# Performance work log

Measured on AMD Instinct MI355X. Metric: run time of the kernel, lower is better.

Reference implementation:

```python
import jax, jax.numpy as jnp
import numpy as np

B, C, H, W = 128, 512, 14, 14
WIN, SHIFT = 7, 3
HEADS, HD = 16, 32
HID = 2048
EPS = 1e-5
N = WIN * WIN
NWH = H // WIN
NW = NWH * NWH


def _rel_pos_index():
    coords = np.stack(np.meshgrid(np.arange(WIN), np.arange(WIN), indexing='ij'))  # (2,Wh,Ww)
    flat = coords.reshape(2, -1)
    rel = (flat[:, :, None] - flat[:, None, :]).transpose(1, 2, 0)  # (N,N,2)
    rel[..., 0] += WIN - 1
    rel[..., 1] += WIN - 1
    rel[..., 0] *= 2 * WIN - 1
    return rel.sum(-1)  # (N,N) in [0, (2W-1)^2)


def _attn_mask():
    img = np.zeros((H, W))
    cnt = 0
    for h in (slice(0, -WIN), slice(-WIN, -SHIFT), slice(-SHIFT, None)):
        for w in (slice(0, -WIN), slice(-WIN, -SHIFT), slice(-SHIFT, None)):
            img[h, w] = cnt
            cnt += 1
    mw = img.reshape(NWH, WIN, NWH, WIN).transpose(0, 2, 1, 3).reshape(-1, N)  # (nW,N)
    d = mw[:, None, :] - mw[:, :, None]
    return np.where(d != 0, -100.0, 0.0).astype(np.float32)  # (nW,N,N)


REL_IDX = _rel_pos_index()
ATTN_MASK = jnp.asarray(_attn_mask())


def _ln_c(x, w, b):
    # LayerNorm2d: normalize over channel dim of NCHW
    mu = x.mean(axis=1, keepdims=True)
    var = ((x - mu) ** 2).mean(axis=1, keepdims=True)
    xn = (x - mu) * jax.lax.rsqrt(var + EPS)
    return xn * w[None, :, None, None] + b[None, :, None, None]


def setup_inputs() -> dict:
    key = jax.random.key(0)
    ks = jax.random.split(key, 12)
    s = 0.02
    return {
        'x': jax.random.normal(ks[0], (B, C, H, W), jnp.float32),
        'ln1_w': jnp.ones((C,), jnp.float32),
        'ln1_b': jnp.zeros((C,), jnp.float32),
        'qkv_w': jax.random.normal(ks[1], (3 * C, C), jnp.float32) * s,
        'qkv_b': jnp.zeros((3 * C,), jnp.float32),
        'rel_bias': jax.random.normal(ks[2], ((2 * WIN - 1) ** 2, HEADS), jnp.float32) * s,
        'proj_w': jax.random.normal(ks[3], (C, C), jnp.float32) * s,
        'proj_b': jnp.zeros((C,), jnp.float32),
        'gamma1': jnp.full((C,), 1e-6, jnp.float32),
        'ln2_w': jnp.ones((C,), jnp.float32),
        'ln2_b': jnp.zeros((C,), jnp.float32),
        'fc1_w': jax.random.normal(ks[4], (HID, C), jnp.float32) * s,
        'fc1_b': jnp.zeros((HID,), jnp.float32),
        'fc2_w': jax.random.normal(ks[5], (C, HID), jnp.float32) * s,
        'fc2_b': jnp.zeros((C,), jnp.float32),
        'gamma2': jnp.full((C,), 1e-6, jnp.float32),
    }


def reference(x, ln1_w, ln1_b, qkv_w, qkv_b, rel_bias, proj_w, proj_b, gamma1,
              ln2_w, ln2_b, fc1_w, fc1_b, fc2_w, fc2_b, gamma2):
    # ---- shifted-window attention branch ----
    y = _ln_c(x, ln1_w, ln1_b).transpose(0, 2, 3, 1)  # (B,H,W,C)
    y = jnp.roll(y, (-SHIFT, -SHIFT), axis=(1, 2))
    # window partition -> (B*nW, N, C)
    xw = y.reshape(B, NWH, WIN, NWH, WIN, C).transpose(0, 1, 3, 2, 4, 5).reshape(B * NW, N, C)
    qkv = (xw @ qkv_w.T + qkv_b).reshape(B * NW, N, 3, HEADS, HD).transpose(2, 0, 3, 1, 4)
    q, k, v = qkv[0], qkv[1], qkv[2]  # (B*nW, heads, N, hd)
    attn = jnp.einsum('bhnd,bhmd->bhnm', q * (HD ** -0.5), k)
    bias = rel_bias[REL_IDX.reshape(-1)].reshape(N, N, HEADS).transpose(2, 0, 1)  # (heads,N,N)
    attn = attn + bias[None]
    attn = attn.reshape(B, NW, HEADS, N, N) + ATTN_MASK[None, :, None]
    attn = jax.nn.softmax(attn.reshape(B * NW, HEADS, N, N), axis=-1)
    out = jnp.einsum('bhnm,bhmd->bhnd', attn, v).transpose(0, 2, 1, 3).reshape(B * NW, N, C)
    out = out @ proj_w.T + proj_b
    # window reverse + roll back
    y = out.reshape(B, NWH, NWH, WIN, WIN, C).transpose(0, 1, 3, 2, 4, 5).reshape(B, H, W, C)
    y = jnp.roll(y, (SHIFT, SHIFT), axis=(1, 2))
    y = gamma1 * y  # layer scale over channel (last dim in NHWC)
    x = x + y.transpose(0, 3, 1, 2)
    # ---- MLP branch ----
    z = _ln_c(x, ln2_w, ln2_b).transpose(0, 2, 3, 1)  # (B,H,W,C)
    z = jax.nn.gelu(z @ fc1_w.T + fc1_b, approximate=False)
    z = z @ fc2_w.T + fc2_b
    z = gamma2 * z
    return x + z.transpose(0, 3, 1, 2)
```

## Files before the change

kernel.cpp:

```cpp
#include <hip/hip_runtime.h>
#include <cmath>
#include <cstdint>

typedef float floatx4 __attribute__((ext_vector_type(4)));

#define EPS_ 1e-5f
#define QSCALE 0.17677669529663689f

__device__ __forceinline__ void gload16(const uint8_t* g, uint8_t* l) {
  __builtin_amdgcn_global_load_lds(
      (const __attribute__((address_space(1))) void*)g,
      (__attribute__((address_space(3))) void*)l, 16, 0, 0);
}

template<bool HI>
__device__ __forceinline__ int pk_fp8(float a, float b, int old) {
  return __builtin_amdgcn_cvt_pk_fp8_f32(a, b, old, HI);
}
__device__ __forceinline__ int pk_fp8x4(float v0, float v1, float v2, float v3) {
  int w = pk_fp8<false>(v0, v1, 0);
  return pk_fp8<true>(v2, v3, w);
}

__device__ __forceinline__ uint16_t f2bf(float f) {
  uint32_t u = __float_as_uint(f);
  return (uint16_t)((u + 0x7fffu + ((u >> 16) & 1u)) >> 16);
}
__device__ __forceinline__ float bf2f(uint16_t h) {
  return __uint_as_float(((uint32_t)h) << 16);
}


template<int K>
__global__ void cvt_frag(const float* __restrict__ s, uint8_t* __restrict__ d, int n4) {
  const int i = blockIdx.x * 256 + threadIdx.x;
  if (i >= n4) return;
  const int kq = K >> 2;
  const int n = i / kq;
  const int k = (i - n * kq) << 2;
  const float4 v = ((const float4*)s)[i];
  const int panel = ((n >> 6) << 2) + (n & 3);
  const int lm = (n >> 2) & 15;
  const long addr = (long)panel * (16 * K) + ((k >> 3) << 7) + (lm << 3) + (k & 4);
  *(int*)(d + addr) = pk_fp8x4(v.x, v.y, v.z, v.w);
}

__global__ __launch_bounds__(256)
void ln_stats_nchw(const float* __restrict__ x, float* __restrict__ mu, float* __restrict__ rs) {
  const int tl = threadIdx.x & 63;
  const int wv = threadIdx.x >> 6;
  const int t = blockIdx.x * 64 + tl;
  const int b = t / 196;
  const int p = t - b * 196;
  const float* xp = x + (long)b * 100352 + p;
  float s = 0.f, ss = 0.f;
  const int cbeg = wv * 128;
  for (int c = cbeg; c < cbeg + 128; ++c) {
    const float v = xp[(long)c * 196];
    s += v; ss += v * v;
  }
  __shared__ float sb[4][64], qb[4][64];
  sb[wv][tl] = s; qb[wv][tl] = ss;
  __syncthreads();
  if (wv == 0) {
    s  = sb[0][tl] + sb[1][tl] + sb[2][tl] + sb[3][tl];
    ss = qb[0][tl] + qb[1][tl] + qb[2][tl] + qb[3][tl];
    const float m = s * (1.f / 512.f);
    const float var = ss * (1.f / 512.f) - m * m;
    mu[t] = m;
    rs[t] = rsqrtf(var + EPS_);
  }
}

__global__ __launch_bounds__(256)
void ln1_apply(const float* __restrict__ x, const float* __restrict__ mu, const float* __restrict__ rs,
               const float* __restrict__ w, const float* __restrict__ bb, uint8_t* __restrict__ A) {
  __shared__ float tile[64][53];
  const int bid = blockIdx.x;
  const int ct = bid & 7;
  const int pt = (bid >> 3) & 3;
  const int b = bid >> 5;
  const int p0 = pt * 49, c0 = ct * 64;
  const long xbase = (long)b * 100352;
  for (int idx = threadIdx.x; idx < 3136; idx += 256) {
    const int cl = idx / 49;
    const int pl = idx - cl * 49;
    tile[cl][pl] = x[xbase + (long)(c0 + cl) * 196 + p0 + pl];
  }
  __syncthreads();
  const int tbase = b * 196 + p0;
  for (int idx = threadIdx.x; idx < 784; idx += 256) {
    const int pl = idx >> 4;
    const int cq = (idx & 15) << 2;
    const int t = tbase + pl;
    const int c = c0 + cq;
    const float m = mu[t], rr = rs[t];
    const float v0 = (tile[cq + 0][pl] - m) * rr * w[c + 0] + bb[c + 0];
    const float v1 = (tile[cq + 1][pl] - m) * rr * w[c + 1] + bb[c + 1];
    const float v2 = (tile[cq + 2][pl] - m) * rr * w[c + 2] + bb[c + 2];
    const float v3 = (tile[cq + 3][pl] - m) * rr * w[c + 3] + bb[c + 3];
    const long addr = (long)(t & ~15) * 512 + ((c >> 3) << 7) + ((t & 15) << 3) + (c & 4);
    *(int*)(A + addr) = pk_fp8x4(v0, v1, v2, v3);
  }
}

__global__ __launch_bounds__(256)
void ln2_panel(const uint16_t* __restrict__ Xb, const float* __restrict__ S1,
               const float* __restrict__ S2, const float* __restrict__ w,
               const float* __restrict__ bb, uint8_t* __restrict__ Z) {
  __shared__ float xs[16 * 516];
  const int p = blockIdx.x;
  const int t0 = p * 16;
  for (int idx = threadIdx.x; idx < 1024; idx += 256) {
    const int tl = idx >> 6;
    const int c8 = (idx & 63) << 3;
    const uint4 raw = *(const uint4*)(Xb + ((long)(t0 + tl) << 9) + c8);
    float* xr = xs + tl * 516 + c8;
    xr[0] = bf2f((uint16_t)(raw.x & 0xffff)); xr[1] = bf2f((uint16_t)(raw.x >> 16));
    xr[2] = bf2f((uint16_t)(raw.y & 0xffff)); xr[3] = bf2f((uint16_t)(raw.y >> 16));
    xr[4] = bf2f((uint16_t)(raw.z & 0xffff)); xr[5] = bf2f((uint16_t)(raw.z >> 16));
    xr[6] = bf2f((uint16_t)(raw.w & 0xffff)); xr[7] = bf2f((uint16_t)(raw.w >> 16));
  }
  __syncthreads();
  uint8_t* zp = Z + (long)p * 8192;
  for (int e = threadIdx.x; e < 2048; e += 256) {
    const int off = e << 2;
    const int k8 = off >> 7;
    const int tl = (off >> 3) & 15;
    const int c = (k8 << 3) + (off & 4);
    const int t = t0 + tl;
    const float m = S1[t] * (1.f / 512.f);
    const float var = S2[t] * (1.f / 512.f) - m * m;
    const float r = rsqrtf(var + EPS_);
    const float* xr = xs + tl * 516 + c;
    const float v0 = (xr[0] - m) * r * w[c + 0] + bb[c + 0];
    const float v1 = (xr[1] - m) * r * w[c + 1] + bb[c + 1];
    const float v2 = (xr[2] - m) * r * w[c + 2] + bb[c + 2];
    const float v3 = (xr[3] - m) * r * w[c + 3] + bb[c + 3];
    *(int*)(zp + off) = pk_fp8x4(v0, v1, v2, v3);
  }
}

template<int MI, int K, int EPI, int NG, int T>
__global__ __launch_bounds__(256)
void gemm_bl(const uint8_t* __restrict__ A, const uint8_t* __restrict__ Bw,
             const float* __restrict__ bias, const float* __restrict__ res,
             const uint16_t* __restrict__ resb, const float* __restrict__ gamma,
             uint8_t* __restrict__ outb, float* __restrict__ outf,
             uint16_t* __restrict__ outh, float* __restrict__ S1, float* __restrict__ S2,
             const int N) {
  const int kx = blockIdx.x & 7;
  const int sx = blockIdx.x >> 3;
  const int t = (sx / NG) * 8 + kx;
  if (t >= T) return;
  const int g = sx - (sx / NG) * NG;
  __shared__ uint8_t Bs[33280];
  const int tid = threadIdx.x;
  const int wave = tid >> 6, lane = tid & 63;
  const int lm = lane & 15, lq = lane >> 4;
  const long m0 = (long)t * (MI * 64);
  const long n0 = (long)g << 6;
  const uint8_t* abase = A + (m0 + wave * MI * 16) * (long)K + (lane << 3);
  floatx4 acc[MI][4] = {};
  constexpr int NKS = K / 32;
  long aC[MI], aN[MI];
  #pragma unroll
  for (int i = 0; i < MI; ++i) aC[i] = *(const long*)(abase + (long)i * 16 * K);
  #pragma unroll
  for (int ph = 0; ph < K / 512; ++ph) {
    const uint8_t* bsrc = Bw + n0 * K + ph * 8192;
    #pragma unroll
    for (int j = 0; j < 4; ++j)
      #pragma unroll
      for (int c = 0; c < 2; ++c)
        gload16(bsrc + (long)j * 16 * K + c * 4096 + tid * 16,
                Bs + j * 8192 + c * 4096 + tid * 16);
    __syncthreads();
    #pragma unroll
    for (int ksl = 0; ksl < 16; ++ksl) {
      const int sg = ph * 16 + ksl;
      if (sg + 1 < NKS) {
        #pragma unroll
        for (int i = 0; i < MI; ++i)
          aN[i] = *(const long*)(abase + (long)i * 16 * K + (sg + 1) * 512);
      }
      long bf[4];
      #pragma unroll
      for (int j = 0; j < 4; ++j)
        bf[j] = *(const long*)(Bs + j * 8192 + ksl * 512 + (lane << 3));
      #pragma unroll
      for (int i = 0; i < MI; ++i)
        #pragma unroll
        for (int j = 0; j < 4; ++j)
          acc[i][j] = __builtin_amdgcn_mfma_f32_16x16x32_fp8_fp8(aC[i], bf[j], acc[i][j], 0, 0, 0);
      #pragma unroll
      for (int i = 0; i < MI; ++i) aC[i] = aN[i];
    }
    if (K / 512 > 1 && ph + 1 < K / 512) __syncthreads();
  }
  const int cb = (g << 6) + (lm << 2);
  const float4 b4 = *(const float4*)(bias + cb);
  float4 g4 = make_float4(0.f, 0.f, 0.f, 0.f);
  if (EPI == 1 || EPI == 3) g4 = *(const float4*)(gamma + cb);
  const float qs = (EPI == 0 && cb < 512) ? QSCALE : 1.f;
  if (EPI != 3) {
    #pragma unroll
    for (int i = 0; i < MI; ++i) {
      #pragma unroll
      for (int r = 0; r < 4; ++r) {
        const long rowg = m0 + wave * MI * 16 + i * 16 + lq * 4 + r;
        float v0 = acc[i][0][r] + b4.x;
        float v1 = acc[i][1][r] + b4.y;
        float v2 = acc[i][2][r] + b4.z;
        float v3 = acc[i][3][r] + b4.w;
        if (EPI == 0) {
          *(int*)(outb + rowg * (long)N + cb) = pk_fp8x4(v0 * qs, v1 * qs, v2 * qs, v3 * qs);
        } else if (EPI == 2) {
          v0 = 0.5f * v0 * (1.f + erff(v0 * 0.70710678118654752f));
          v1 = 0.5f * v1 * (1.f + erff(v1 * 0.70710678118654752f));
          v2 = 0.5f * v2 * (1.f + erff(v2 * 0.70710678118654752f));
          v3 = 0.5f * v3 * (1.f + erff(v3 * 0.70710678118654752f));
          const long addr = (rowg & ~15L) * 2048 + ((cb >> 3) << 7) + ((rowg & 15) << 3) + (cb & 4);
          *(int*)(outb + addr) = pk_fp8x4(v0, v1, v2, v3);
        } else {
          const unsigned rg = (unsigned)rowg;
          const unsigned bi = rg / 196u;
          const unsigned p = rg - bi * 196u;
          const float* xr = res + (long)bi * 100352 + p;
          const float o0 = xr[(long)(cb + 0) * 196] + g4.x * v0;
          const float o1 = xr[(long)(cb + 1) * 196] + g4.y * v1;
          const float o2 = xr[(long)(cb + 2) * 196] + g4.z * v2;
          const float o3 = xr[(long)(cb + 3) * 196] + g4.w * v3;
          ushort4 hv;
          hv.x = f2bf(o0); hv.y = f2bf(o1); hv.z = f2bf(o2); hv.w = f2bf(o3);
          *(ushort4*)(outh + rowg * 512 + cb) = hv;
          const float q0 = bf2f(hv.x), q1 = bf2f(hv.y), q2 = bf2f(hv.z), q3 = bf2f(hv.w);
          float s = q0 + q1 + q2 + q3;
          float ss = q0 * q0 + q1 * q1 + q2 * q2 + q3 * q3;
          s += __shfl_xor(s, 1);  ss += __shfl_xor(ss, 1);
          s += __shfl_xor(s, 2);  ss += __shfl_xor(ss, 2);
          s += __shfl_xor(s, 4);  ss += __shfl_xor(ss, 4);
          s += __shfl_xor(s, 8);  ss += __shfl_xor(ss, 8);
          if (lm == 0) {
            atomicAdd(S1 + rowg, s);
            atomicAdd(S2 + rowg, ss);
          }
        }
      }
    }
  } else {
    float* Tx = (float*)Bs;
    __syncthreads();
    #pragma unroll
    for (int i = 0; i < MI; ++i) {
      #pragma unroll
      for (int r = 0; r < 4; ++r) {
        const long rowg = m0 + wave * MI * 16 + i * 16 + lq * 4 + r;
        const int rl = (int)(rowg - m0);
        const ushort4 rb = *(const ushort4*)(resb + rowg * 512 + cb);
        Tx[(lm * 4 + 0) * 129 + rl] = bf2f(rb.x) + g4.x * (acc[i][0][r] + b4.x);
        Tx[(lm * 4 + 1) * 129 + rl] = bf2f(rb.y) + g4.y * (acc[i][1][r] + b4.y);
        Tx[(lm * 4 + 2) * 129 + rl] = bf2f(rb.z) + g4.z * (acc[i][2][r] + b4.z);
        Tx[(lm * 4 + 3) * 129 + rl] = bf2f(rb.w) + g4.w * (acc[i][3][r] + b4.w);
      }
    }
    __syncthreads();
    #pragma unroll
    for (int t2 = 0; t2 < 32; ++t2) {
      const int idx = t2 * 256 + tid;
      const int rl = idx & 127;
      const int ch = idx >> 7;
      const unsigned m = (unsigned)(m0 + rl);
      const unsigned bi = m / 196u;
      const unsigned p = m - bi * 196u;
      outf[(long)bi * 100352 + (long)(n0 + ch) * 196 + p] = Tx[ch * 129 + rl];
    }
  }
}

__global__ __launch_bounds__(256)
void bm_build(const float* __restrict__ rel_bias, float* __restrict__ BM) {
  const int hw = blockIdx.x;
  const int head = hw >> 2, wpos = hw & 3;
  const int wi = wpos >> 1, wj = wpos & 1;
  for (int k = 0; k < 4; ++k) {
    const int idx = k * 256 + threadIdx.x;
    const int tile = idx >> 6, l = idx & 63;
    const int qi = tile >> 2, ti = tile & 3;
    const int n = l & 15, g = l >> 4;
    const int query = qi * 16 + n;
    const int qy = query / 7, qx = query - qy * 7;
    const int hh = wi * 7 + qy, ww = wj * 7 + qx;
    const int ri = (hh < 7 ? 0 : (hh < 11 ? 1 : 2)) * 3 + (ww < 7 ? 0 : (ww < 11 ? 1 : 2));
    float4 ov;
    float vv[4];
    #pragma unroll
    for (int r = 0; r < 4; ++r) {
      const int key = ti * 16 + g * 4 + r;
      float v;
      if (query >= 49 || key >= 49) {
        v = -3.0e38f;
      } else {
        const int ky = key / 7, kx = key - ky * 7;
        const int bidx = (qy - ky + 6) * 13 + (qx - kx + 6);
        const int h2 = wi * 7 + ky, w2 = wj * 7 + kx;
        const int rj = (h2 < 7 ? 0 : (h2 < 11 ? 1 : 2)) * 3 + (w2 < 7 ? 0 : (w2 < 11 ? 1 : 2));
        v = rel_bias[bidx * 16 + head] + ((ri != rj) ? -100.f : 0.f);
      }
      vv[r] = v;
    }
    ov.x = vv[0]; ov.y = vv[1]; ov.z = vv[2]; ov.w = vv[3];
    *(float4*)(BM + ((long)(hw * 16 + tile) << 8) + l * 4) = ov;
  }
}

__device__ __forceinline__ void tr4(const uint32_t d[4], uint32_t o[4]) {
  #pragma unroll
  for (int c = 0; c < 4; ++c)
    o[c] = ((d[0] >> (8 * c)) & 0xffu) | (((d[1] >> (8 * c)) & 0xffu) << 8)
         | (((d[2] >> (8 * c)) & 0xffu) << 16) | (((d[3] >> (8 * c)) & 0xffu) << 24);
}

__global__ __launch_bounds__(256)
void attn_mfma(const uint8_t* __restrict__ QKV, const float* __restrict__ BM,
               uint8_t* __restrict__ AT) {
  __shared__ uint8_t lds[4][9984];
  const int wave = threadIdx.x >> 6, lane = threadIdx.x & 63;
  const int n = lane & 15, g = lane >> 4;
  const int gw = blockIdx.x * 4 + wave;
  const int wd = gw >> 4, head = gw & 15;
  const int b = wd >> 2, wpos = wd & 3;
  const int wi = wpos >> 1, wj = wpos & 1;
  uint8_t* Pb = lds[wave];
  uint8_t* Vt = lds[wave] + 4608;
  uint8_t* Ot = lds[wave] + 6912;
  const long base = (long)b * 196 * 1536;
  auto tok = [&](int slot) -> int {
    const int ty = slot / 7, tx = slot - ty * 7;
    int h = wi * 7 + ty + 3; if (h >= 14) h -= 14;
    int w = wj * 7 + tx + 3; if (w >= 14) w -= 14;
    return h * 14 + w;
  };
  long Ak[4], Bq[4];
  #pragma unroll
  for (int t4 = 0; t4 < 4; ++t4) {
    int slot = t4 * 16 + n; if (slot > 48) slot = 48;
    const long tb = base + (long)tok(slot) * 1536 + head * 32 + g * 8;
    Bq[t4] = *(const long*)(QKV + tb);
    Ak[t4] = *(const long*)(QKV + tb + 512);
  }
  #pragma unroll
  for (int bb2 = 0; bb2 < 2; ++bb2) {
    const int blk = lane + bb2 * 64;
    const int dq = blk >> 4, tq = blk & 15;
    uint32_t d4[4], o4[4];
    #pragma unroll
    for (int r = 0; r < 4; ++r) {
      int slot = tq * 4 + r; if (slot > 48) slot = 48;
      d4[r] = *(const uint32_t*)(QKV + base + (long)tok(slot) * 1536 + 1024 + head * 32 + dq * 4);
    }
    tr4(d4, o4);
    #pragma unroll
    for (int c = 0; c < 4; ++c)
      *(uint32_t*)(Vt + (dq * 4 + c) * 72 + tq * 4) = o4[c];
  }
  floatx4 acc[4][4];
  const float* bmw = BM + ((long)(head * 4 + wpos) << 12) + lane * 4;
  #pragma unroll
  for (int qi = 0; qi < 4; ++qi)
    #pragma unroll
    for (int ti = 0; ti < 4; ++ti) {
      const float4 bv = *(const float4*)(bmw + ((qi * 4 + ti) << 8));
      acc[qi][ti][0] = bv.x; acc[qi][ti][1] = bv.y;
      acc[qi][ti][2] = bv.z; acc[qi][ti][3] = bv.w;
    }
  #pragma unroll
  for (int qi = 0; qi < 4; ++qi)
    #pragma unroll
    for (int ti = 0; ti < 4; ++ti)
      acc[qi][ti] = __builtin_amdgcn_mfma_f32_16x16x32_fp8_fp8(Ak[ti], Bq[qi], acc[qi][ti], 0, 0, 0);
  #pragma unroll
  for (int qi = 0; qi < 4; ++qi) {
    float mx = -3.0e38f;
    #pragma unroll
    for (int ti = 0; ti < 4; ++ti)
      #pragma unroll
      for (int r = 0; r < 4; ++r) mx = fmaxf(mx, acc[qi][ti][r]);
    mx = fmaxf(mx, __shfl_xor(mx, 16));
    mx = fmaxf(mx, __shfl_xor(mx, 32));
    float sum = 0.f;
    #pragma unroll
    for (int ti = 0; ti < 4; ++ti)
      #pragma unroll
      for (int r = 0; r < 4; ++r) {
        const float e = __expf(acc[qi][ti][r] - mx);
        acc[qi][ti][r] = e; sum += e;
      }
    sum += __shfl_xor(sum, 16);
    sum += __shfl_xor(sum, 32);
    const float inv = 1.f / sum;
    #pragma unroll
    for (int ti = 0; ti < 4; ++ti) {
      const int pw = pk_fp8x4(acc[qi][ti][0] * inv, acc[qi][ti][1] * inv,
                              acc[qi][ti][2] * inv, acc[qi][ti][3] * inv);
      *(uint32_t*)(Pb + (qi * 16 + n) * 72 + ti * 16 + g * 4) = pw;
    }
  }
  asm volatile("s_waitcnt lgkmcnt(0)" ::: "memory");
  long Bv[2][2];
  #pragma unroll
  for (int ni = 0; ni < 2; ++ni)
    #pragma unroll
    for (int s = 0; s < 2; ++s)
      Bv[ni][s] = *(const long*)(Vt + (ni * 16 + n) * 72 + s * 32 + g * 8);
  floatx4 o[4][2] = {};
  #pragma unroll
  for (int qi = 0; qi < 4; ++qi)
    #pragma unroll
    for (int s = 0; s < 2; ++s) {
      const long Ap = *(const long*)(Pb + (qi * 16 + n) * 72 + s * 32 + g * 8);
      #pragma unroll
      for (int ni = 0; ni < 2; ++ni)
        o[qi][ni] = __builtin_amdgcn_mfma_f32_16x16x32_fp8_fp8(Ap, Bv[ni][s], o[qi][ni], 0, 0, 0);
    }
  #pragma unroll
  for (int qi = 0; qi < 4; ++qi)
    #pragma unroll
    for (int ni = 0; ni < 2; ++ni)
      #pragma unroll
      for (int r = 0; r < 4; ++r)
        Ot[(qi * 16 + g * 4 + r) * 48 + ni * 16 + n] =
            (uint8_t)(pk_fp8<false>(o[qi][ni][r], 0.f, 0) & 0xff);
  asm volatile("s_waitcnt lgkmcnt(0)" ::: "memory");
  if (lane < 49) {
    const int m = b * 196 + tok(lane);
    uint8_t* opb = AT + (long)(m & ~15) * 512 + ((m & 15) << 3);
    #pragma unroll
    for (int d8 = 0; d8 < 4; ++d8)
      *(long*)(opb + (head * 4 + d8) * 128) = *(const long*)(Ot + lane * 48 + d8 * 8);
  }
}

extern "C" void kernel_launch(void* const* d_in, const int* in_sizes, int n_in,
                              void* d_out, int out_size, void* d_ws, size_t ws_size,
                              hipStream_t stream) {
  const float* x      = (const float*)d_in[0];
  const float* ln1_w  = (const float*)d_in[1];
  const float* ln1_b  = (const float*)d_in[2];
  const float* qkv_w  = (const float*)d_in[3];
  const float* qkv_b  = (const float*)d_in[4];
  const float* relb   = (const float*)d_in[5];
  const float* proj_w = (const float*)d_in[6];
  const float* proj_b = (const float*)d_in[7];
  const float* gamma1 = (const float*)d_in[8];
  const float* ln2_w  = (const float*)d_in[9];
  const float* ln2_b  = (const float*)d_in[10];
  const float* fc1_w  = (const float*)d_in[11];
  const float* fc1_b  = (const float*)d_in[12];
  const float* fc2_w  = (const float*)d_in[13];
  const float* fc2_b  = (const float*)d_in[14];
  const float* gamma2 = (const float*)d_in[15];
  float* out = (float*)d_out;
  char* ws = (char*)d_ws;

  float*    mu1 = (float*)(ws + 0);
  float*    rs1 = (float*)(ws + 100352);
  float*    S1  = (float*)(ws + 200704);
  float*    S2  = (float*)(ws + 301056);
  uint8_t*  Wq  = (uint8_t*)(ws + 401408);
  uint8_t*  Wp  = (uint8_t*)(ws + 1187840);
  uint8_t*  W1  = (uint8_t*)(ws + 1449984);
  uint8_t*  W2  = (uint8_t*)(ws + 2498560);
  float*    BMt = (float*)  (ws + 3547136);
  uint8_t*  Afp = (uint8_t*)(ws + 4595712);
  uint16_t* X1b = (uint16_t*)(ws + 68820992);
  uint8_t*  QKV = (uint8_t*)(ws + 120201216);
  uint8_t*  AT  = (uint8_t*)(ws + 158736384);
  uint8_t*  Hb  = (uint8_t*)(ws + 120201216);

  hipMemsetAsync(ws + 200704, 0, 200704, stream);

  cvt_frag<512> <<<768,  256, 0, stream>>>(qkv_w, Wq, 196608);
  cvt_frag<512> <<<256,  256, 0, stream>>>(proj_w, Wp, 65536);
  cvt_frag<512> <<<1024, 256, 0, stream>>>(fc1_w, W1, 262144);
  cvt_frag<2048><<<1024, 256, 0, stream>>>(fc2_w, W2, 262144);
  bm_build<<<64, 256, 0, stream>>>(relb, BMt);

  ln_stats_nchw<<<392, 256, 0, stream>>>(x, mu1, rs1);
  ln1_apply<<<4096, 256, 0, stream>>>(x, mu1, rs1, ln1_w, ln1_b, Afp);

  gemm_bl<4, 512, 0, 24, 98><<<2496, 256, 0, stream>>>(Afp, Wq, qkv_b, nullptr, nullptr, nullptr, QKV, nullptr, nullptr, nullptr, nullptr, 1536);

  attn_mfma<<<2048, 256, 0, stream>>>(QKV, BMt, AT);

  gemm_bl<4, 512, 1, 8, 98><<<832, 256, 0, stream>>>(AT, Wp, proj_b, x, nullptr, gamma1, nullptr, nullptr, X1b, S1, S2, 512);

  ln2_panel<<<1568, 256, 0, stream>>>(X1b, S1, S2, ln2_w, ln2_b, Afp);

  gemm_bl<4, 512, 2, 32, 98><<<3328, 256, 0, stream>>>(Afp, W1, fc1_b, nullptr, nullptr, nullptr, Hb, nullptr, nullptr, nullptr, nullptr, 2048);
  gemm_bl<2, 2048, 3, 8, 196><<<1600, 256, 0, stream>>>(Hb, W2, fc2_b, nullptr, X1b, gamma2, nullptr, out, nullptr, nullptr, nullptr, 512);
}
```

Measured before the change: 406.4 us.

## Deepen A-operand prefetch, raise MFMA priority, and use sigmoid GELU in GEMM

The fp8 GEMM now prefetches A fragments two k-steps ahead using ping-pong registers instead of one step, to hide global load latency. MFMA issue is wrapped in s_setprio. Launch bounds request 4 blocks per CU and shared memory is shrunk for non-residual epilogues to aid occupancy. The exact erf GELU in the fc1 epilogue is replaced with the x*sigmoid(1.702x) approximation, cutting epilogue ALU cost but deviating from the exact GELU numerics.

```diff
diff --git a/kernel.cpp b/kernel.cpp
--- a/kernel.cpp
+++ b/kernel.cpp
@@ -28,6 +28,11 @@
 }
 __device__ __forceinline__ float bf2f(uint16_t h) {
   return __uint_as_float(((uint32_t)h) << 16);
+}
+
+__device__ __forceinline__ float fast_gelu(float v) {
+  const float t = __expf(-1.702f * v);
+  return v * __builtin_amdgcn_rcpf(1.f + t);
 }
 
 
@@ -142,7 +147,7 @@
 }
 
 template<int MI, int K, int EPI, int NG, int T>
-__global__ __launch_bounds__(256)
+__global__ __launch_bounds__(256, 4)
 void gemm_bl(const uint8_t* __restrict__ A, const uint8_t* __restrict__ Bw,
              const float* __restrict__ bias, const float* __restrict__ res,
              const uint16_t* __restrict__ resb, const float* __restrict__ gamma,
@@ -154,7 +159,7 @@
   const int t = (sx / NG) * 8 + kx;
   if (t >= T) return;
   const int g = sx - (sx / NG) * NG;
-  __shared__ uint8_t Bs[33280];
+  __shared__ __align__(16) uint8_t Bs[(EPI == 3) ? 33280 : 32768];
   const int tid = threadIdx.x;
   const int wave = tid >> 6, lane = tid & 63;
   const int lm = lane & 15, lq = lane >> 4;
@@ -163,9 +168,12 @@
   const uint8_t* abase = A + (m0 + wave * MI * 16) * (long)K + (lane << 3);
   floatx4 acc[MI][4] = {};
   constexpr int NKS = K / 32;
-  long aC[MI], aN[MI];
-  #pragma unroll
-  for (int i = 0; i < MI; ++i) aC[i] = *(const long*)(abase + (long)i * 16 * K);
+  long aP0[MI], aP1[MI];
+  #pragma unroll
+  for (int i = 0; i < MI; ++i) {
+    aP0[i] = *(const long*)(abase + (long)i * 16 * K);
+    aP1[i] = *(const long*)(abase + (long)i * 16 * K + 512);
+  }
   #pragma unroll
   for (int ph = 0; ph < K / 512; ++ph) {
     const uint8_t* bsrc = Bw + n0 * K + ph * 8192;
@@ -179,22 +187,27 @@
     #pragma unroll
     for (int ksl = 0; ksl < 16; ++ksl) {
       const int sg = ph * 16 + ksl;
-      if (sg + 1 < NKS) {
+      long aC[MI];
+      #pragma unroll
+      for (int i = 0; i < MI; ++i) aC[i] = (ksl & 1) ? aP1[i] : aP0[i];
+      if (sg + 2 < NKS) {
         #pragma unroll
-        for (int i = 0; i < MI; ++i)
-          aN[i] = *(const long*)(abase + (long)i * 16 * K + (sg + 1) * 512);
+        for (int i = 0; i < MI; ++i) {
+          const long v = *(const long*)(abase + (long)i * 16 * K + (long)(sg + 2) * 512);
+          if (ksl & 1) aP1[i] = v; else aP0[i] = v;
+        }
       }
       long bf[4];
       #pragma unroll
       for (int j = 0; j < 4; ++j)
         bf[j] = *(const long*)(Bs + j * 8192 + ksl * 512 + (lane << 3));
+      __builtin_amdgcn_s_setprio(1);
       #pragma unroll
       for (int i = 0; i < MI; ++i)
         #pragma unroll
         for (int j = 0; j < 4; ++j)
           acc[i][j] = __builtin_amdgcn_mfma_f32_16x16x32_fp8_fp8(aC[i], bf[j], acc[i][j], 0, 0, 0);
-      #pragma unroll
-      for (int i = 0; i < MI; ++i) aC[i] = aN[i];
+      __builtin_amdgcn_s_setprio(0);
     }
     if (K / 512 > 1 && ph + 1 < K / 512) __syncthreads();
   }
@@ -216,10 +229,10 @@
         if (EPI == 0) {
           *(int*)(outb + rowg * (long)N + cb) = pk_fp8x4(v0 * qs, v1 * qs, v2 * qs, v3 * qs);
         } else if (EPI == 2) {
-          v0 = 0.5f * v0 * (1.f + erff(v0 * 0.70710678118654752f));
-          v1 = 0.5f * v1 * (1.f + erff(v1 * 0.70710678118654752f));
-          v2 = 0.5f * v2 * (1.f + erff(v2 * 0.70710678118654752f));
-          v3 = 0.5f * v3 * (1.f + erff(v3 * 0.70710678118654752f));
+          v0 = fast_gelu(v0);
+          v1 = fast_gelu(v1);
+          v2 = fast_gelu(v2);
+          v3 = fast_gelu(v3);
           const long addr = (rowg & ~15L) * 2048 + ((cb >> 3) << 7) + ((rowg & 15) << 3) + (cb & 4);
           *(int*)(outb + addr) = pk_fp8x4(v0, v1, v2, v3);
         } else {
```

Result: faster. 388.1 us (-4.5%).
